# Kernel optimization log

Measured on AMD Instinct MI355X. Metric: run time of the kernel, lower is better.

## Reference

```python
import jax, jax.numpy as jnp
import numpy as np

N = 8192
F_IN = 64
F_OUT = 64
ALPHA = 0.2  # LeakyReLU negative slope
NEG_INF = -9e15


def setup_inputs() -> dict:
    key = jax.random.key(0)
    k1, k2, k3, k4 = jax.random.split(key, 4)
    h = jax.random.normal(k1, (N, F_IN), dtype=jnp.float32)
    adj = jax.random.randint(k2, (N, N), 0, 2, dtype=jnp.int32)
    W = jax.random.normal(k3, (F_OUT, F_IN), dtype=jnp.float32) * (1.0 / np.sqrt(F_IN))
    a = jax.random.normal(k4, (2 * F_OUT,), dtype=jnp.float32) * (1.0 / np.sqrt(2 * F_OUT))
    return {"h": h, "adj": adj, "W": W, "a": a}


def reference(h, adj, W, a):
    # Wh = h @ W.T  (nn.Linear with no bias)
    Wh = h @ W.T  # [N, F_out]
    # The original builds [N*N, 2F] pairs then applies `a`; this is exactly
    # e_ij = leakyrelu(a1 . Wh_i + a2 . Wh_j) -- decomposed form, same math.
    a1, a2 = a[:F_OUT], a[F_OUT:]
    src = Wh @ a1  # [N]
    dst = Wh @ a2  # [N]
    e = jax.nn.leaky_relu(src[:, None] + dst[None, :], negative_slope=ALPHA)  # [N, N]
    scores = jnp.where(adj > 0, e, NEG_INF)
    attention = jax.nn.softmax(scores, axis=1)
    # dropout is identity in eval mode (dropout=0.0)
    h_prime = attention @ Wh  # [N, F_out]
    return jax.nn.elu(h_prime)
```

## Files before the change

### kernel.cpp

```cpp
#include <hip/hip_runtime.h>
#include <hip/hip_bf16.h>

#define NN 8192
#define F 64
#define ALPHA 0.2f
#define L2E 1.44269504f
#define DBOUND 16.0f
#define G 8
#define COLS (NN / G)
#define NSTEPS (COLS / 32)

typedef __attribute__((ext_vector_type(8))) short short8;
typedef __attribute__((ext_vector_type(4))) float f32x4;
typedef __attribute__((ext_vector_type(4))) int i32x4;

__device__ __forceinline__ unsigned fb(float x) {
    return __builtin_bit_cast(unsigned, x);
}
__device__ __forceinline__ short f2bf(float x) {
    union { float f; unsigned u; } v; v.f = x;
    unsigned r = v.u + 0x7FFF + ((v.u >> 16) & 1);
    return (short)(r >> 16);
}

__global__ __launch_bounds__(256) void k_prep(const float* __restrict__ h,
        const float* __restrict__ W, const float* __restrict__ a,
        short* __restrict__ WhTt, float* __restrict__ src, float* __restrict__ dst2) {
    __shared__ float Wl[F][F + 1];
    __shared__ short shT[F][4];
    int tid = threadIdx.x;
    for (int m = 0; m < 4; ++m) {
        int idx = m * 1024 + tid * 4;
        float4 v = *(const float4*)&W[idx];
        int row = idx >> 6, col = idx & 63;
        Wl[row][col] = v.x; Wl[row][col + 1] = v.y;
        Wl[row][col + 2] = v.z; Wl[row][col + 3] = v.w;
    }
    __syncthreads();
    int w = tid >> 6, lane = tid & 63;
    int i = blockIdx.x * 4 + w;
    const float* hrow = &h[(size_t)i * F];
    float wh = 0.f;
    #pragma unroll
    for (int k = 0; k < F; k += 4) {
        float4 hv = *(const float4*)&hrow[k];
        wh += hv.x * Wl[lane][k] + hv.y * Wl[lane][k + 1]
            + hv.z * Wl[lane][k + 2] + hv.w * Wl[lane][k + 3];
    }
    shT[lane][w] = f2bf(wh);
    float s1 = wh * a[lane];
    float s2 = wh * a[F + lane];
    #pragma unroll
    for (int off = 32; off; off >>= 1) {
        s1 += __shfl_xor(s1, off);
        s2 += __shfl_xor(s2, off);
    }
    if (lane == 0) { src[i] = s1; dst2[i] = s2 * L2E; }
    __syncthreads();
    if (tid < F) {
        int f = tid;
        int b = blockIdx.x;
        int t = b >> 3;
        int off = (b * 4) & 31;
        size_t addr = (((size_t)(t * 4 + (f >> 4)) * 64
                       + (off >> 3) * 16 + (f & 15)) << 3) + (off & 7);
        short4 v = make_short4(shT[f][0], shT[f][1], shT[f][2], shT[f][3]);
        *(short4*)&WhTt[addr] = v;
    }
}

__global__ __launch_bounds__(256) void k_mask(const int* __restrict__ adj,
                                              unsigned long long* __restrict__ mg) {
    int w = threadIdx.x >> 6, l = threadIdx.x & 63;
    int gw = blockIdx.x * 4 + w;
    const int NW = 2048 * 4;
    const int NCH = (NN * NN) / 256;
    int sh = 4 * (l & 15);
    #pragma unroll 4
    for (int c = gw; c < NCH; c += NW) {
        size_t base = (size_t)c * 256;
        i32x4 a = __builtin_nontemporal_load((const i32x4*)(adj + base) + l);
        unsigned n = (a.x > 0 ? 1u : 0u) | (a.y > 0 ? 2u : 0u)
                   | (a.z > 0 ? 4u : 0u) | (a.w > 0 ? 8u : 0u);
        unsigned long long v = (unsigned long long)n << sh;
        v |= __shfl_xor(v, 1);
        v |= __shfl_xor(v, 2);
        v |= __shfl_xor(v, 4);
        v |= __shfl_xor(v, 8);
        if ((l & 15) == 0)
            mg[base / 64 + (l >> 4)] = v;
    }
}

__global__ __launch_bounds__(256, 4) void k_attn(const unsigned* __restrict__ maskg,
        const short8* __restrict__ WhTt, const float* __restrict__ src,
        const float* __restrict__ dst2,
        float* __restrict__ Opart, float* __restrict__ lpart) {
    __shared__ unsigned mlds[64][33];
    __shared__ float dlds[COLS];

    int rb = blockIdx.x / G;
    int g  = blockIdx.x % G;
    int jbase = g * COLS;
    int tid = threadIdx.x;

    for (int idx = tid; idx < 64 * (COLS / 32); idx += 256) {
        int rr = idx >> 5, cc = idx & 31;
        mlds[rr][cc] = maskg[(size_t)(rb * 64 + rr) * (NN / 32) + (jbase >> 5) + cc];
    }
    for (int idx = tid; idx < COLS; idx += 256)
        dlds[idx] = dst2[jbase + idx];
    __syncthreads();

    int w = tid >> 6, lane = tid & 63;
    int r = lane & 15, q = lane >> 4;
    int qs = q * 8;
    int i = rb * 64 + w * 16 + r;

    float srcv = src[i];
    float sM = srcv + DBOUND;
    float Mi = fmaxf(sM, ALPHA * sM);
    float sL  = srcv * L2E;
    float MiL = Mi * L2E;
    float C1 = sL - MiL;
    float C2 = fmaf(sL, ALPHA, -MiL);

    f32x4 acc0{}, acc1{}, acc2{}, acc3{}, acc4{};
    short8 ones;
    #pragma unroll
    for (int k = 0; k < 8; ++k) ones[k] = (short)0x3F80;

    const unsigned* mrow = &mlds[w * 16 + r][0];

#define LDB(tt, B0, B1, B2, B3) { \
    const short8* bp = WhTt + (size_t)(g * 32 + (tt)) * 256; \
    B0 = bp[lane]; B1 = bp[64 + lane]; B2 = bp[128 + lane]; B3 = bp[192 + lane]; }

#define PEL(dv, bit, eo) { \
    float t1 = (dv) + C1; \
    float t2 = fmaf((dv), ALPHA, C2); \
    float e = __builtin_amdgcn_exp2f(fmaxf(t1, t2)); \
    eo = (bit) ? e : 0.0f; }

    short8 cb0, cb1, cb2, cb3, nb0, nb1, nb2, nb3;
    LDB(0, cb0, cb1, cb2, cb3)
    unsigned cm = mrow[0];
    float4 cd0 = *(const float4*)&dlds[qs];
    float4 cd1 = *(const float4*)&dlds[qs + 4];

    #pragma unroll 4
    for (int t = 0; t < NSTEPS; ++t) {
        int tn = (t + 1 < NSTEPS) ? t + 1 : t;
        LDB(tn, nb0, nb1, nb2, nb3)

        unsigned nm = mrow[tn];
        float4 nd0 = *(const float4*)&dlds[tn * 32 + qs];
        float4 nd1 = *(const float4*)&dlds[tn * 32 + qs + 4];

        unsigned m8 = (cm >> qs) & 0xffu;
        float e0, e1, e2, e3, e4, e5, e6, e7;
        PEL(cd0.x, (m8 & 1u),   e0) PEL(cd0.y, (m8 & 2u),   e1)
        PEL(cd0.z, (m8 & 4u),   e2) PEL(cd0.w, (m8 & 8u),   e3)
        PEL(cd1.x, (m8 & 16u),  e4) PEL(cd1.y, (m8 & 32u),  e5)
        PEL(cd1.z, (m8 & 64u),  e6) PEL(cd1.w, (m8 & 128u), e7)

        unsigned w0 = __builtin_amdgcn_perm(fb(e1), fb(e0), 0x07060302u);
        unsigned w1 = __builtin_amdgcn_perm(fb(e3), fb(e2), 0x07060302u);
        unsigned w2 = __builtin_amdgcn_perm(fb(e5), fb(e4), 0x07060302u);
        unsigned w3 = __builtin_amdgcn_perm(fb(e7), fb(e6), 0x07060302u);
        short8 af = __builtin_bit_cast(short8, make_uint4(w0, w1, w2, w3));

        acc0 = __builtin_amdgcn_mfma_f32_16x16x32_bf16(af, cb0, acc0, 0, 0, 0);
        acc1 = __builtin_amdgcn_mfma_f32_16x16x32_bf16(af, cb1, acc1, 0, 0, 0);
        acc2 = __builtin_amdgcn_mfma_f32_16x16x32_bf16(af, cb2, acc2, 0, 0, 0);
        acc3 = __builtin_amdgcn_mfma_f32_16x16x32_bf16(af, cb3, acc3, 0, 0, 0);
        acc4 = __builtin_amdgcn_mfma_f32_16x16x32_bf16(af, ones, acc4, 0, 0, 0);

        cb0 = nb0; cb1 = nb1; cb2 = nb2; cb3 = nb3;
        cm = nm; cd0 = nd0; cd1 = nd1;
    }
#undef PEL
#undef LDB

    int ic = rb * 64 + w * 16 + q * 4;
    if (r == 0) {
        #pragma unroll
        for (int reg = 0; reg < 4; ++reg)
            lpart[(size_t)g * NN + ic + reg] = acc4[reg];
    }

    size_t ob = (size_t)g * (size_t)(NN * F);
    #pragma unroll
    for (int reg = 0; reg < 4; ++reg) {
        size_t ro = ob + (size_t)(ic + reg) * F + r;
        Opart[ro]      = acc0[reg];
        Opart[ro + 16] = acc1[reg];
        Opart[ro + 32] = acc2[reg];
        Opart[ro + 48] = acc3[reg];
    }
}

__global__ __launch_bounds__(256) void k_reduce(const float* __restrict__ Opart,
        const float* __restrict__ lpart, float* __restrict__ out) {
    int idx = blockIdx.x * 256 + threadIdx.x;
    int i = idx >> 6;
    float o = 0.f, l = 0.f;
    #pragma unroll
    for (int g = 0; g < G; ++g) {
        o += Opart[(size_t)g * (NN * F) + idx];
        l += lpart[(size_t)g * NN + i];
    }
    float hp = o / l;
    out[idx] = hp > 0.f ? hp : __expf(hp) - 1.f;
}

extern "C" void kernel_launch(void* const* d_in, const int* in_sizes, int n_in,
                              void* d_out, int out_size, void* d_ws, size_t ws_size,
                              hipStream_t stream) {
    const float* h  = (const float*)d_in[0];
    const int* adj  = (const int*)d_in[1];
    const float* W  = (const float*)d_in[2];
    const float* a  = (const float*)d_in[3];
    float* out = (float*)d_out;

    char* ws = (char*)d_ws;
    const size_t OFF_WHTT = 0;
    const size_t OFF_SRC  = (1u << 20);
    const size_t OFF_DST  = OFF_SRC + (32u << 10);
    const size_t OFF_LP   = OFF_DST + (32u << 10);
    const size_t OFF_MASK = OFF_LP + (size_t)G * NN * 4;
    const size_t OFF_OP   = OFF_MASK + (size_t)NN * (NN / 8);

    short* WhTt  = (short*)(ws + OFF_WHTT);
    float* src   = (float*)(ws + OFF_SRC);
    float* dst2  = (float*)(ws + OFF_DST);
    float* lpart = (float*)(ws + OFF_LP);
    unsigned long long* maskg = (unsigned long long*)(ws + OFF_MASK);
    float* Opart = (float*)(ws + OFF_OP);

    k_mask<<<2048, 256, 0, stream>>>(adj, maskg);
    k_prep<<<NN / 4, 256, 0, stream>>>(h, W, a, WhTt, src, dst2);
    k_attn<<<(NN / 64) * G, 256, 0, stream>>>((const unsigned*)maskg,
                                              (const short8*)WhTt, src, dst2,
                                              Opart, lpart);
    k_reduce<<<(NN * F) / 256, 256, 0, stream>>>(Opart, lpart, out);
}
```

Before: 89.68 us.

## Split mask build by column halves and overlap attention on low half with mask of high half

The adjacency bitmask build is split into two column halves. A first kernel packs columns 0-4095. A mixed kernel then interleaves attention blocks for column groups 0-3 with mask-packing blocks for columns 4096-8191, and a last kernel runs attention for groups 4-7. The goal is to overlap the bandwidth-bound mask conversion with the compute-bound attention MFMA work. In exchange there is an extra launch, and the mixed kernel's LDS allocation and launch bounds apply to its mask blocks too, which may limit how many run at once.

Result: slower. 112.2 us (+25.1%).

```diff
diff --git a/kernel.cpp b/kernel.cpp
--- a/kernel.cpp
+++ b/kernel.cpp
@@ -21,6 +21,133 @@
     union { float f; unsigned u; } v; v.f = x;
     unsigned r = v.u + 0x7FFF + ((v.u >> 16) & 1);
     return (short)(r >> 16);
+}
+
+__device__ __forceinline__ void mask_body(const int* __restrict__ adj,
+        unsigned long long* __restrict__ mg, int colbase, int gw, int l) {
+    int sh = 4 * (l & 15);
+    #pragma unroll 4
+    for (int k = 0; k < 16; ++k) {
+        int cid = gw + k * 8192;
+        int rr = cid >> 4, cc = cid & 15;
+        size_t base = (size_t)rr * NN + colbase + cc * 256;
+        i32x4 av = __builtin_nontemporal_load((const i32x4*)(adj + base) + l);
+        unsigned n = (av.x > 0 ? 1u : 0u) | (av.y > 0 ? 2u : 0u)
+                   | (av.z > 0 ? 4u : 0u) | (av.w > 0 ? 8u : 0u);
+        unsigned long long v = (unsigned long long)n << sh;
+        v |= __shfl_xor(v, 1);
+        v |= __shfl_xor(v, 2);
+        v |= __shfl_xor(v, 4);
+        v |= __shfl_xor(v, 8);
+        if ((l & 15) == 0)
+            mg[base / 64 + (l >> 4)] = v;
+    }
+}
+
+__device__ __forceinline__ void attn_body(int rb, int g,
+        const unsigned* __restrict__ maskg, const short8* __restrict__ WhTt,
+        const float* __restrict__ src, const float* __restrict__ dst2,
+        float* __restrict__ Opart, float* __restrict__ lpart) {
+    __shared__ unsigned mlds[64][33];
+    __shared__ float dlds[COLS];
+
+    int jbase = g * COLS;
+    int tid = threadIdx.x;
+
+    for (int idx = tid; idx < 64 * (COLS / 32); idx += 256) {
+        int rr = idx >> 5, cc = idx & 31;
+        mlds[rr][cc] = maskg[(size_t)(rb * 64 + rr) * (NN / 32) + (jbase >> 5) + cc];
+    }
+    for (int idx = tid; idx < COLS; idx += 256)
+        dlds[idx] = dst2[jbase + idx];
+    __syncthreads();
+
+    int w = tid >> 6, lane = tid & 63;
+    int r = lane & 15, q = lane >> 4;
+    int qs = q * 8;
+    int i = rb * 64 + w * 16 + r;
+
+    float srcv = src[i];
+    float sM = srcv + DBOUND;
+    float Mi = fmaxf(sM, ALPHA * sM);
+    float sL  = srcv * L2E;
+    float MiL = Mi * L2E;
+    float C1 = sL - MiL;
+    float C2 = fmaf(sL, ALPHA, -MiL);
+
+    f32x4 acc0{}, acc1{}, acc2{}, acc3{}, acc4{};
+    short8 ones;
+    #pragma unroll
+    for (int k = 0; k < 8; ++k) ones[k] = (short)0x3F80;
+
+    const unsigned* mrow = &mlds[w * 16 + r][0];
+
+#define LDB(tt, B0, B1, B2, B3) { \
+    const short8* bp = WhTt + (size_t)(g * 32 + (tt)) * 256; \
+    B0 = bp[lane]; B1 = bp[64 + lane]; B2 = bp[128 + lane]; B3 = bp[192 + lane]; }
+
+#define PEL(dv, bit, eo) { \
+    float t1 = (dv) + C1; \
+    float t2 = fmaf((dv), ALPHA, C2); \
+    float e = __builtin_amdgcn_exp2f(fmaxf(t1, t2)); \
+    eo = (bit) ? e : 0.0f; }
+
+    short8 cb0, cb1, cb2, cb3, nb0, nb1, nb2, nb3;
+    LDB(0, cb0, cb1, cb2, cb3)
+    unsigned cm = mrow[0];
+    float4 cd0 = *(const float4*)&dlds[qs];
+    float4 cd1 = *(const float4*)&dlds[qs + 4];
+
+    #pragma unroll 4
+    for (int t = 0; t < NSTEPS; ++t) {
+        int tn = (t + 1 < NSTEPS) ? t + 1 : t;
+        LDB(tn, nb0, nb1, nb2, nb3)
+
+        unsigned nm = mrow[tn];
+        float4 nd0 = *(const float4*)&dlds[tn * 32 + qs];
+        float4 nd1 = *(const float4*)&dlds[tn * 32 + qs + 4];
+
+        unsigned m8 = (cm >> qs) & 0xffu;
+        float e0, e1, e2, e3, e4, e5, e6, e7;
+        PEL(cd0.x, (m8 & 1u),   e0) PEL(cd0.y, (m8 & 2u),   e1)
+        PEL(cd0.z, (m8 & 4u),   e2) PEL(cd0.w, (m8 & 8u),   e3)
+        PEL(cd1.x, (m8 & 16u),  e4) PEL(cd1.y, (m8 & 32u),  e5)
+        PEL(cd1.z, (m8 & 64u),  e6) PEL(cd1.w, (m8 & 128u), e7)
+
+        unsigned w0 = __builtin_amdgcn_perm(fb(e1), fb(e0), 0x07060302u);
+        unsigned w1 = __builtin_amdgcn_perm(fb(e3), fb(e2), 0x07060302u);
+        unsigned w2 = __builtin_amdgcn_perm(fb(e5), fb(e4), 0x07060302u);
+        unsigned w3 = __builtin_amdgcn_perm(fb(e7), fb(e6), 0x07060302u);
+        short8 af = __builtin_bit_cast(short8, make_uint4(w0, w1, w2, w3));
+
+        acc0 = __builtin_amdgcn_mfma_f32_16x16x32_bf16(af, cb0, acc0, 0, 0, 0);
+        acc1 = __builtin_amdgcn_mfma_f32_16x16x32_bf16(af, cb1, acc1, 0, 0, 0);
+        acc2 = __builtin_amdgcn_mfma_f32_16x16x32_bf16(af, cb2, acc2, 0, 0, 0);
+        acc3 = __builtin_amdgcn_mfma_f32_16x16x32_bf16(af, cb3, acc3, 0, 0, 0);
+        acc4 = __builtin_amdgcn_mfma_f32_16x16x32_bf16(af, ones, acc4, 0, 0, 0);
+
+        cb0 = nb0; cb1 = nb1; cb2 = nb2; cb3 = nb3;
+        cm = nm; cd0 = nd0; cd1 = nd1;
+    }
+#undef PEL
+#undef LDB
+
+    int ic = rb * 64 + w * 16 + q * 4;
+    if (r == 0) {
+        #pragma unroll
+        for (int reg = 0; reg < 4; ++reg)
+            lpart[(size_t)g * NN + ic + reg] = acc4[reg];
+    }
+
+    size_t ob = (size_t)g * (size_t)(NN * F);
+    #pragma unroll
+    for (int reg = 0; reg < 4; ++reg) {
+        size_t ro = ob + (size_t)(ic + reg) * F + r;
+        Opart[ro]      = acc0[reg];
+        Opart[ro + 16] = acc1[reg];
+        Opart[ro + 32] = acc2[reg];
+        Opart[ro + 48] = acc3[reg];
+    }
 }
 
 __global__ __launch_bounds__(256) void k_prep(const float* __restrict__ h,
@@ -69,135 +196,35 @@
     }
 }
 
-__global__ __launch_bounds__(256) void k_mask(const int* __restrict__ adj,
-                                              unsigned long long* __restrict__ mg) {
+__global__ __launch_bounds__(256) void k_mask_lo(const int* __restrict__ adj,
+                                                 unsigned long long* __restrict__ mg) {
     int w = threadIdx.x >> 6, l = threadIdx.x & 63;
-    int gw = blockIdx.x * 4 + w;
-    const int NW = 2048 * 4;
-    const int NCH = (NN * NN) / 256;
-    int sh = 4 * (l & 15);
-    #pragma unroll 4
-    for (int c = gw; c < NCH; c += NW) {
-        size_t base = (size_t)c * 256;
-        i32x4 a = __builtin_nontemporal_load((const i32x4*)(adj + base) + l);
-        unsigned n = (a.x > 0 ? 1u : 0u) | (a.y > 0 ? 2u : 0u)
-                   | (a.z > 0 ? 4u : 0u) | (a.w > 0 ? 8u : 0u);
-        unsigned long long v = (unsigned long long)n << sh;
-        v |= __shfl_xor(v, 1);
-        v |= __shfl_xor(v, 2);
-        v |= __shfl_xor(v, 4);
-        v |= __shfl_xor(v, 8);
-        if ((l & 15) == 0)
-            mg[base / 64 + (l >> 4)] = v;
-    }
-}
-
-__global__ __launch_bounds__(256, 4) void k_attn(const unsigned* __restrict__ maskg,
+    mask_body(adj, mg, 0, blockIdx.x * 4 + w, l);
+}
+
+__global__ __launch_bounds__(256, 4) void k_mix(const int* __restrict__ adj,
+        unsigned long long* __restrict__ mg,
         const short8* __restrict__ WhTt, const float* __restrict__ src,
         const float* __restrict__ dst2,
         float* __restrict__ Opart, float* __restrict__ lpart) {
-    __shared__ unsigned mlds[64][33];
-    __shared__ float dlds[COLS];
-
-    int rb = blockIdx.x / G;
-    int g  = blockIdx.x % G;
-    int jbase = g * COLS;
-    int tid = threadIdx.x;
-
-    for (int idx = tid; idx < 64 * (COLS / 32); idx += 256) {
-        int rr = idx >> 5, cc = idx & 31;
-        mlds[rr][cc] = maskg[(size_t)(rb * 64 + rr) * (NN / 32) + (jbase >> 5) + cc];
-    }
-    for (int idx = tid; idx < COLS; idx += 256)
-        dlds[idx] = dst2[jbase + idx];
-    __syncthreads();
-
-    int w = tid >> 6, lane = tid & 63;
-    int r = lane & 15, q = lane >> 4;
-    int qs = q * 8;
-    int i = rb * 64 + w * 16 + r;
-
-    float srcv = src[i];
-    float sM = srcv + DBOUND;
-    float Mi = fmaxf(sM, ALPHA * sM);
-    float sL  = srcv * L2E;
-    float MiL = Mi * L2E;
-    float C1 = sL - MiL;
-    float C2 = fmaf(sL, ALPHA, -MiL);
-
-    f32x4 acc0{}, acc1{}, acc2{}, acc3{}, acc4{};
-    short8 ones;
-    #pragma unroll
-    for (int k = 0; k < 8; ++k) ones[k] = (short)0x3F80;
-
-    const unsigned* mrow = &mlds[w * 16 + r][0];
-
-#define LDB(tt, B0, B1, B2, B3) { \
-    const short8* bp = WhTt + (size_t)(g * 32 + (tt)) * 256; \
-    B0 = bp[lane]; B1 = bp[64 + lane]; B2 = bp[128 + lane]; B3 = bp[192 + lane]; }
-
-#define PEL(dv, bit, eo) { \
-    float t1 = (dv) + C1; \
-    float t2 = fmaf((dv), ALPHA, C2); \
-    float e = __builtin_amdgcn_exp2f(fmaxf(t1, t2)); \
-    eo = (bit) ? e : 0.0f; }
-
-    short8 cb0, cb1, cb2, cb3, nb0, nb1, nb2, nb3;
-    LDB(0, cb0, cb1, cb2, cb3)
-    unsigned cm = mrow[0];
-    float4 cd0 = *(const float4*)&dlds[qs];
-    float4 cd1 = *(const float4*)&dlds[qs + 4];
-
-    #pragma unroll 4
-    for (int t = 0; t < NSTEPS; ++t) {
-        int tn = (t + 1 < NSTEPS) ? t + 1 : t;
-        LDB(tn, nb0, nb1, nb2, nb3)
-
-        unsigned nm = mrow[tn];
-        float4 nd0 = *(const float4*)&dlds[tn * 32 + qs];
-        float4 nd1 = *(const float4*)&dlds[tn * 32 + qs + 4];
-
-        unsigned m8 = (cm >> qs) & 0xffu;
-        float e0, e1, e2, e3, e4, e5, e6, e7;
-        PEL(cd0.x, (m8 & 1u),   e0) PEL(cd0.y, (m8 & 2u),   e1)
-        PEL(cd0.z, (m8 & 4u),   e2) PEL(cd0.w, (m8 & 8u),   e3)
-        PEL(cd1.x, (m8 & 16u),  e4) PEL(cd1.y, (m8 & 32u),  e5)
-        PEL(cd1.z, (m8 & 64u),  e6) PEL(cd1.w, (m8 & 128u), e7)
-
-        unsigned w0 = __builtin_amdgcn_perm(fb(e1), fb(e0), 0x07060302u);
-        unsigned w1 = __builtin_amdgcn_perm(fb(e3), fb(e2), 0x07060302u);
-        unsigned w2 = __builtin_amdgcn_perm(fb(e5), fb(e4), 0x07060302u);
-        unsigned w3 = __builtin_amdgcn_perm(fb(e7), fb(e6), 0x07060302u);
-        short8 af = __builtin_bit_cast(short8, make_uint4(w0, w1, w2, w3));
-
-        acc0 = __builtin_amdgcn_mfma_f32_16x16x32_bf16(af, cb0, acc0, 0, 0, 0);
-        acc1 = __builtin_amdgcn_mfma_f32_16x16x32_bf16(af, cb1, acc1, 0, 0, 0);
-        acc2 = __builtin_amdgcn_mfma_f32_16x16x32_bf16(af, cb2, acc2, 0, 0, 0);
-        acc3 = __builtin_amdgcn_mfma_f32_16x16x32_bf16(af, cb3, acc3, 0, 0, 0);
-        acc4 = __builtin_amdgcn_mfma_f32_16x16x32_bf16(af, ones, acc4, 0, 0, 0);
-
-        cb0 = nb0; cb1 = nb1; cb2 = nb2; cb3 = nb3;
-        cm = nm; cd0 = nd0; cd1 = nd1;
-    }
-#undef PEL
-#undef LDB
-
-    int ic = rb * 64 + w * 16 + q * 4;
-    if (r == 0) {
-        #pragma unroll
-        for (int reg = 0; reg < 4; ++reg)
-            lpart[(size_t)g * NN + ic + reg] = acc4[reg];
-    }
-
-    size_t ob = (size_t)g * (size_t)(NN * F);
-    #pragma unroll
-    for (int reg = 0; reg < 4; ++reg) {
-        size_t ro = ob + (size_t)(ic + reg) * F + r;
-        Opart[ro]      = acc0[reg];
-        Opart[ro + 16] = acc1[reg];
-        Opart[ro + 32] = acc2[reg];
-        Opart[ro + 48] = acc3[reg];
-    }
+    int b = blockIdx.x;
+    if (b % 5 == 0) {
+        int aid = b / 5;
+        attn_body(aid >> 2, aid & 3, (const unsigned*)mg, WhTt, src, dst2,
+                  Opart, lpart);
+    } else {
+        int mid = b - b / 5 - 1;
+        int w = threadIdx.x >> 6, l = threadIdx.x & 63;
+        mask_body(adj, mg, 4096, mid * 4 + w, l);
+    }
+}
+
+__global__ __launch_bounds__(256, 4) void k_attn_hi(const unsigned* __restrict__ maskg,
+        const short8* __restrict__ WhTt, const float* __restrict__ src,
+        const float* __restrict__ dst2,
+        float* __restrict__ Opart, float* __restrict__ lpart) {
+    attn_body(blockIdx.x >> 2, 4 + (blockIdx.x & 3), maskg, WhTt, src, dst2,
+              Opart, lpart);
 }
 
 __global__ __launch_bounds__(256) void k_reduce(const float* __restrict__ Opart,
@@ -238,10 +265,11 @@
     unsigned long long* maskg = (unsigned long long*)(ws + OFF_MASK);
     float* Opart = (float*)(ws + OFF_OP);
 
-    k_mask<<<2048, 256, 0, stream>>>(adj, maskg);
     k_prep<<<NN / 4, 256, 0, stream>>>(h, W, a, WhTt, src, dst2);
-    k_attn<<<(NN / 64) * G, 256, 0, stream>>>((const unsigned*)maskg,
-                                              (const short8*)WhTt, src, dst2,
-                                              Opart, lpart);
+    k_mask_lo<<<2048, 256, 0, stream>>>(adj, maskg);
+    k_mix<<<2560, 256, 0, stream>>>(adj, maskg, (const short8*)WhTt, src, dst2,
+                                    Opart, lpart);
+    k_attn_hi<<<512, 256, 0, stream>>>((const unsigned*)maskg, (const short8*)WhTt,
+                                       src, dst2, Opart, lpart);
     k_reduce<<<(NN * F) / 256, 256, 0, stream>>>(Opart, lpart, out);
 }
```
